# Performance work log

Hardware: AMD Instinct MI355X
Metric: run time of the kernel (lower is better)

## Reference

```python
import jax, jax.numpy as jnp
import numpy as np

N_NODES = 100000
N_EDGES = 2500000


def setup_inputs() -> dict:
    key = jax.random.key(0)
    ks = jax.random.split(key, 13)
    inp = {
        "x": jax.random.normal(ks[0], (N_NODES, 4), dtype=jnp.float32),
        "edge_index": jax.random.randint(ks[1], (2, N_EDGES), 0, N_NODES, dtype=jnp.int64),
        "W_fc1": jax.random.normal(ks[2], (4, 32), dtype=jnp.float32) * 0.5,
        "b_fc1": jax.random.normal(ks[3], (32,), dtype=jnp.float32) * 0.1,
        "W_c1": jax.random.normal(ks[4], (32, 32), dtype=jnp.float32) * (1.0 / np.sqrt(32)),
        "b_c1": jax.random.normal(ks[5], (32,), dtype=jnp.float32) * 0.1,
        "W_c2": jax.random.normal(ks[6], (32, 32), dtype=jnp.float32) * (1.0 / np.sqrt(32)),
        "b_c2": jax.random.normal(ks[7], (32,), dtype=jnp.float32) * 0.1,
        "W_c3": jax.random.normal(ks[8], (32, 32), dtype=jnp.float32) * (1.0 / np.sqrt(32)),
        "b_c3": jax.random.normal(ks[9], (32,), dtype=jnp.float32) * 0.1,
        "W_fc2": jax.random.normal(ks[10], (32, 3), dtype=jnp.float32) * (1.0 / np.sqrt(32)),
        "b_fc2": jax.random.normal(ks[11], (3,), dtype=jnp.float32) * 0.1,
    }
    return inp


def _gcn_norm(edge_index, n_nodes):
    # PyG GCNConv default: add self-loops, symmetric normalization deg^-1/2 A_hat deg^-1/2
    src = jnp.concatenate([edge_index[0], jnp.arange(n_nodes, dtype=edge_index.dtype)])
    dst = jnp.concatenate([edge_index[1], jnp.arange(n_nodes, dtype=edge_index.dtype)])
    deg = jax.ops.segment_sum(jnp.ones_like(dst, dtype=jnp.float32), dst, num_segments=n_nodes)
    dinv = jnp.where(deg > 0, jax.lax.rsqrt(deg), 0.0)
    norm = dinv[src] * dinv[dst]  # [E + N]
    return src, dst, norm


def _gcn_conv(x, src, dst, norm, W, b, n_nodes):
    h = x @ W                                  # [N, 32] small GEMM
    msg = h[src] * norm[:, None]               # gather + scale  [E+N, 32]
    out = jax.ops.segment_sum(msg, dst, num_segments=n_nodes)  # scatter-add
    return out + b


def reference(x, edge_index, W_fc1, b_fc1, W_c1, b_c1, W_c2, b_c2, W_c3, b_c3, W_fc2, b_fc2):
    n_nodes = x.shape[0]
    src, dst, norm = _gcn_norm(edge_index, n_nodes)
    h = jax.nn.relu(x @ W_fc1 + b_fc1)
    h = jax.nn.relu(_gcn_conv(h, src, dst, norm, W_c1, b_c1, n_nodes))
    h = jax.nn.relu(_gcn_conv(h, src, dst, norm, W_c2, b_c2, n_nodes))
    h = jax.nn.relu(_gcn_conv(h, src, dst, norm, W_c3, b_c3, n_nodes))
    return h @ W_fc2 + b_fc2
```

## Files before the change

kernel.cpp:

```cpp
#include <hip/hip_runtime.h>
#include <hip/hip_fp16.h>


constexpr int N_NODES = 100000;
constexpr int N_EDGES = 2500000;
constexpr int QDIV    = 25000;
constexpr int BUCKET  = 256;
constexpr int NBUCK   = (N_NODES + BUCKET - 1) / BUCKET;
constexpr int NBLK    = 512;
constexpr int CHUNK   = (N_EDGES + NBLK - 1) / NBLK;
constexpr int SCAP    = 8192;
constexpr int PERLANE = NBLK / 64;

__global__ __launch_bounds__(256) void k_binfill(const int* __restrict__ ei,
                                                 int* __restrict__ binned,
                                                 int* __restrict__ blkbin,
                                                 int* __restrict__ locoff) {
    __shared__ int cnt[NBUCK];
    __shared__ int cur[NBUCK];
    __shared__ int wsum[4];
    __shared__ int stage[CHUNK];
    __shared__ int payload[CHUNK];
    __shared__ unsigned short binv[CHUNK];
    int tid = threadIdx.x;
    int blk = blockIdx.x;
    int beg = blk * CHUNK;
    int end = min(beg + CHUNK, N_EDGES);
    int m = end - beg;

    for (int i = tid; i < NBUCK; i += 256) cnt[i] = 0;
    __syncthreads();
    for (int e = beg + tid; e < end; e += 256) {
        int sv = ei[e];
        int d  = ei[N_EDGES + e];
        int bin = d >> 8;
        atomicAdd(&cnt[bin], 1);
        int i = e - beg;
        payload[i] = (sv << 8) | (d & 255);
        binv[i] = (unsigned short)bin;
    }
    __syncthreads();

    int c0 = (2 * tid     < NBUCK) ? cnt[2 * tid]     : 0;
    int c1 = (2 * tid + 1 < NBUCK) ? cnt[2 * tid + 1] : 0;
    int s  = c0 + c1;
    int incl = s;
#pragma unroll
    for (int o = 1; o < 64; o <<= 1) {
        int tm = __shfl_up(incl, o);
        if ((tid & 63) >= o) incl += tm;
    }
    if ((tid & 63) == 63) wsum[tid >> 6] = incl;
    __syncthreads();
    int wexcl = 0;
#pragma unroll
    for (int wi = 0; wi < 4; ++wi) wexcl += (wi < (tid >> 6)) ? wsum[wi] : 0;
    int texcl = wexcl + incl - s;
    {
        int i = 2 * tid;
        if (i < NBUCK) {
            cur[i] = texcl;
            blkbin[i * NBLK + blk] = c0;
            locoff[blk * NBUCK + i] = beg + texcl;
        }
        i = 2 * tid + 1;
        if (i < NBUCK) {
            int e1 = texcl + c0;
            cur[i] = e1;
            blkbin[i * NBLK + blk] = c1;
            locoff[blk * NBUCK + i] = beg + e1;
        }
    }
    __syncthreads();

    for (int i = tid; i < m; i += 256) {
        int pos = atomicAdd(&cur[binv[i]], 1);
        stage[pos] = payload[i];
    }
    __syncthreads();
    for (int i = tid; i < m; i += 256) binned[beg + i] = stage[i];
}

__global__ __launch_bounds__(256) void k_binwave(const int* __restrict__ blkbin,
                                                 int* __restrict__ bintot,
                                                 int* __restrict__ blkpos) {
    int w = threadIdx.x >> 6, lane = threadIdx.x & 63;
    int bin = blockIdx.x * 4 + w;
    if (bin >= NBUCK) return;
    int v[PERLANE];
#pragma unroll
    for (int i = 0; i < PERLANE; ++i) v[i] = blkbin[bin * NBLK + lane * PERLANE + i];
    int mysum = 0;
#pragma unroll
    for (int i = 0; i < PERLANE; ++i) mysum += v[i];
    int pre = mysum;
#pragma unroll
    for (int o = 1; o < 64; o <<= 1) {
        int t = __shfl_up(pre, o);
        if (lane >= o) pre += t;
    }
    int excl = pre - mysum;
    int run = excl;
#pragma unroll
    for (int i = 0; i < PERLANE; ++i) {
        blkpos[bin * NBLK + lane * PERLANE + i] = run;
        run += v[i];
    }
    if (lane == 63) bintot[bin] = pre;
}

__global__ __launch_bounds__(512) void k_sortdeg(const int* __restrict__ binned,
                                                 const int* __restrict__ blkbin,
                                                 const int* __restrict__ blkpos,
                                                 const int* __restrict__ locoff,
                                                 const int* __restrict__ bintot,
                                                 unsigned short* __restrict__ csr16,
                                                 int* __restrict__ rowseg,
                                                 float* __restrict__ dinv) {
    __shared__ int stage[SCAP];
    __shared__ unsigned short outs[SCAP];
    __shared__ int runlen[NBLK];
    __shared__ int runpos[NBLK];
    __shared__ int cnt[1024];
    __shared__ int sc[1024];
    __shared__ int cur[1024];
    __shared__ int wred[8];
    __shared__ int wtot[8];
    int t = threadIdx.x;
    int b = blockIdx.x;

    int part = 0;
    for (int i = t; i < b; i += 512) part += bintot[i];
#pragma unroll
    for (int o = 32; o > 0; o >>= 1) part += __shfl_xor(part, o);
    if ((t & 63) == 0) wred[t >> 6] = part;

    if (t < NBLK) {
        runlen[t] = blkbin[b * NBLK + t];
        runpos[t] = blkpos[b * NBLK + t];
    }
    cnt[t] = 0; cnt[t + 512] = 0;
    __syncthreads();

    int beg = 0;
#pragma unroll
    for (int wi = 0; wi < 8; ++wi) beg += wred[wi];
    int end = beg + bintot[b];
    int total = end - beg;
    bool fits = (total <= SCAP);

    if (fits) {
        for (int blk = t; blk < NBLK; blk += 512) {
            int len = runlen[blk];
            int srcp = locoff[blk * NBUCK + b];
            int dstp = runpos[blk];
            int i = 0;
            while (i < len && ((srcp + i) & 3)) { stage[dstp + i] = binned[srcp + i]; ++i; }
            for (; i + 3 < len; i += 4) {
                int4 v = *(const int4*)(binned + srcp + i);
                stage[dstp + i]     = v.x;
                stage[dstp + i + 1] = v.y;
                stage[dstp + i + 2] = v.z;
                stage[dstp + i + 3] = v.w;
            }
            for (; i < len; ++i) stage[dstp + i] = binned[srcp + i];
        }
        __syncthreads();
        for (int k = t; k < total; k += 512) {
            int p = stage[k];
            int key = ((p & 255) << 2) | ((p >> 8) / QDIV);
            atomicAdd(&cnt[key], 1);
        }
    } else {
        for (int blk = t; blk < NBLK; blk += 512) {
            int len = runlen[blk];
            int srcp = locoff[blk * NBUCK + b];
            for (int i = 0; i < len; ++i) {
                int p = binned[srcp + i];
                int key = ((p & 255) << 2) | ((p >> 8) / QDIV);
                atomicAdd(&cnt[key], 1);
            }
        }
    }
    __syncthreads();

    int c0 = cnt[2 * t], c1 = cnt[2 * t + 1];
    int s = c0 + c1;
    int incl = s;
#pragma unroll
    for (int o = 1; o < 64; o <<= 1) {
        int tm = __shfl_up(incl, o);
        if ((t & 63) >= o) incl += tm;
    }
    if ((t & 63) == 63) wtot[t >> 6] = incl;
    __syncthreads();
    int wexcl = 0;
#pragma unroll
    for (int wi = 0; wi < 8; ++wi) wexcl += (wi < (t >> 6)) ? wtot[wi] : 0;
    int texcl = wexcl + incl - s;
    sc[2 * t]     = texcl + c0;
    sc[2 * t + 1] = texcl + s;
    __syncthreads();

#pragma unroll
    for (int slot = 0; slot < 2; ++slot) {
        int k = 2 * t + slot;
        int excl = (slot == 0) ? texcl : (texcl + c0);
        cur[k] = excl;
        int dl = k >> 2, q = k & 3;
        int n = b * BUCKET + dl;
        if (n < N_NODES) {
            rowseg[n * 4 + q] = beg + excl;
            if (q == 0) {
                int deg = sc[k + 3] - excl;
                dinv[n] = rsqrtf((float)(deg + 1));
            }
        }
    }
    if (b == NBUCK - 1 && t == 0) rowseg[(size_t)N_NODES * 4] = end;
    __syncthreads();

    if (fits) {
        for (int k = t; k < total; k += 512) {
            int p = stage[k];
            int src = p >> 8;
            int q = src / QDIV;
            int key = ((p & 255) << 2) | q;
            int pos = atomicAdd(&cur[key], 1);
            outs[pos] = (unsigned short)(src - q * QDIV);
        }
        __syncthreads();
        for (int k = t; k < total; k += 512)
            csr16[beg + k] = outs[k];
    } else {
        for (int blk = t; blk < NBLK; blk += 512) {
            int len = runlen[blk];
            int srcp = locoff[blk * NBUCK + b];
            for (int i = 0; i < len; ++i) {
                int p = binned[srcp + i];
                int src = p >> 8;
                int q = src / QDIV;
                int key = ((p & 255) << 2) | q;
                int pos = atomicAdd(&cur[key], 1);
                csr16[beg + pos] = (unsigned short)(src - q * QDIV);
            }
        }
    }
}

__device__ inline void store_half8(__half* p, const float* v) {
    __half2 h[4];
#pragma unroll
    for (int i = 0; i < 4; ++i)
        h[i] = __floats2half2_rn(v[2 * i], v[2 * i + 1]);
    *(float4*)p = *(float4*)h;
}

__device__ inline void acc_half8(float* acc, float4 raw) {
    __half2* hp = (__half2*)&raw;
#pragma unroll
    for (int i = 0; i < 4; ++i) {
        float2 f = __half22float2(hp[i]);
        acc[2 * i]     += f.x;
        acc[2 * i + 1] += f.y;
    }
}

__global__ __launch_bounds__(256) void k_fc1_conv1(
        const float* __restrict__ x,
        const float* __restrict__ Wfc1, const float* __restrict__ bfc1,
        const float* __restrict__ Wc1, const float* __restrict__ dinv,
        __half* __restrict__ g) {
    __shared__ float  sWf[128];
    __shared__ float  sbf[32];
    __shared__ float4 sW[256];
    if (threadIdx.x < 128) sWf[threadIdx.x] = Wfc1[threadIdx.x];
    if (threadIdx.x < 32)  sbf[threadIdx.x] = bfc1[threadIdx.x];
    sW[threadIdx.x] = ((const float4*)Wc1)[threadIdx.x];
    __syncthreads();

    int n = blockIdx.x * 256 + threadIdx.x;
    if (n >= N_NODES) return;

    float4 xin = *(const float4*)(x + (size_t)n * 4);
    float t[32];
#pragma unroll
    for (int j = 0; j < 32; ++j) {
        float a = fmaf(xin.x, sWf[j], sbf[j]);
        a = fmaf(xin.y, sWf[32 + j], a);
        a = fmaf(xin.z, sWf[64 + j], a);
        a = fmaf(xin.w, sWf[96 + j], a);
        t[j] = fmaxf(a, 0.0f);
    }
    float o[32];
#pragma unroll
    for (int j = 0; j < 32; ++j) o[j] = 0.f;
#pragma unroll
    for (int k = 0; k < 32; ++k) {
        float a = t[k];
#pragma unroll
        for (int q = 0; q < 8; ++q) {
            float4 w = sW[k * 8 + q];
            o[q * 4 + 0] = fmaf(a, w.x, o[q * 4 + 0]);
            o[q * 4 + 1] = fmaf(a, w.y, o[q * 4 + 1]);
            o[q * 4 + 2] = fmaf(a, w.z, o[q * 4 + 2]);
            o[q * 4 + 3] = fmaf(a, w.w, o[q * 4 + 3]);
        }
    }
    float dv = dinv[n];
#pragma unroll
    for (int j = 0; j < 32; ++j) o[j] *= dv;
    __half* gp = g + (size_t)n * 32;
    store_half8(gp,      o);
    store_half8(gp + 8,  o + 8);
    store_half8(gp + 16, o + 16);
    store_half8(gp + 24, o + 24);
}

__device__ inline void gather_seg(int beg, int end, int base,
                                  const unsigned short* __restrict__ csr16,
                                  const __half* __restrict__ gin, int sub, float* acc) {
    int k = beg;
    int stop = beg + ((end - beg) & ~3);
    if (k < stop) {
        int s0 = base + csr16[k],     s1 = base + csr16[k + 1];
        int s2 = base + csr16[k + 2], s3 = base + csr16[k + 3];
        k += 4;
        while (k < stop) {
            float4 r0 = *(const float4*)(gin + (size_t)s0 * 32 + sub * 8);
            float4 r1 = *(const float4*)(gin + (size_t)s1 * 32 + sub * 8);
            float4 r2 = *(const float4*)(gin + (size_t)s2 * 32 + sub * 8);
            float4 r3 = *(const float4*)(gin + (size_t)s3 * 32 + sub * 8);
            s0 = base + csr16[k];     s1 = base + csr16[k + 1];
            s2 = base + csr16[k + 2]; s3 = base + csr16[k + 3];
            acc_half8(acc, r0); acc_half8(acc, r1);
            acc_half8(acc, r2); acc_half8(acc, r3);
            k += 4;
        }
        float4 r0 = *(const float4*)(gin + (size_t)s0 * 32 + sub * 8);
        float4 r1 = *(const float4*)(gin + (size_t)s1 * 32 + sub * 8);
        float4 r2 = *(const float4*)(gin + (size_t)s2 * 32 + sub * 8);
        float4 r3 = *(const float4*)(gin + (size_t)s3 * 32 + sub * 8);
        acc_half8(acc, r0); acc_half8(acc, r1);
        acc_half8(acc, r2); acc_half8(acc, r3);
    }
    for (; k < end; ++k) {
        int s = base + csr16[k];
        float4 r = *(const float4*)(gin + (size_t)s * 32 + sub * 8);
        acc_half8(acc, r);
    }
}

__global__ __launch_bounds__(256) void k_gather_mid(
        const int* __restrict__ rowseg,
        const unsigned short* __restrict__ csr16, const __half* __restrict__ gin,
        const float* __restrict__ dinv,
        const float* __restrict__ b, const float* __restrict__ W,
        __half* __restrict__ gout) {
    __shared__ float sS[64 * 33];
    __shared__ float sW[1024];
    __shared__ float sb[32];
    for (int i = threadIdx.x; i < 1024; i += 256) sW[i] = W[i];
    if (threadIdx.x < 32) sb[threadIdx.x] = b[threadIdx.x];

    int nl = threadIdx.x >> 2;
    int sub = threadIdx.x & 3;
    int n = blockIdx.x * 64 + nl;
    float acc[8];
    if (n < N_NODES) {
        float4 self = *(const float4*)(gin + (size_t)n * 32 + sub * 8);
        {
            __half2* hp = (__half2*)&self;
#pragma unroll
            for (int i = 0; i < 4; ++i) {
                float2 f = __half22float2(hp[i]);
                acc[2 * i] = f.x;
                acc[2 * i + 1] = f.y;
            }
        }
        int4 seg = *(const int4*)(rowseg + (size_t)n * 4);
        int segend = rowseg[(size_t)n * 4 + 4];
        gather_seg(seg.x, seg.y, 0,         csr16, gin, sub, acc);
        gather_seg(seg.y, seg.z, QDIV,      csr16, gin, sub, acc);
        gather_seg(seg.z, seg.w, 2 * QDIV,  csr16, gin, sub, acc);
        gather_seg(seg.w, segend, 3 * QDIV, csr16, gin, sub, acc);
#pragma unroll
        for (int i = 0; i < 8; ++i) sS[nl * 33 + sub * 8 + i] = acc[i];
    }
    __syncthreads();

    if (n >= N_NODES) return;
    float dv = dinv[n];
    float t[32];
#pragma unroll
    for (int kk = 0; kk < 32; ++kk)
        t[kk] = fmaxf(fmaf(dv, sS[nl * 33 + kk], sb[kk]), 0.0f);
    float o[8];
#pragma unroll
    for (int j = 0; j < 8; ++j) o[j] = 0.f;
#pragma unroll
    for (int kk = 0; kk < 32; ++kk) {
        float a = t[kk];
#pragma unroll
        for (int j = 0; j < 8; ++j)
            o[j] = fmaf(a, sW[kk * 32 + sub * 8 + j], o[j]);
    }
#pragma unroll
    for (int j = 0; j < 8; ++j) o[j] *= dv;
    store_half8(gout + (size_t)n * 32 + sub * 8, o);
}

__global__ __launch_bounds__(256) void k_gather_out(
        const int* __restrict__ rowseg,
        const unsigned short* __restrict__ csr16, const __half* __restrict__ gin,
        const float* __restrict__ dinv,
        const float* __restrict__ bc3, const float* __restrict__ Wfc2,
        const float* __restrict__ bfc2, float* __restrict__ out) {
    __shared__ float sS[64 * 33];
    __shared__ float sW[96];
    __shared__ float sb[32];
    __shared__ float sb2[3];
    if (threadIdx.x < 96) sW[threadIdx.x] = Wfc2[threadIdx.x];
    if (threadIdx.x < 32) sb[threadIdx.x] = bc3[threadIdx.x];
    if (threadIdx.x < 3)  sb2[threadIdx.x] = bfc2[threadIdx.x];

    int nl = threadIdx.x >> 2;
    int sub = threadIdx.x & 3;
    int n = blockIdx.x * 64 + nl;
    float acc[8];
    if (n < N_NODES) {
        float4 self = *(const float4*)(gin + (size_t)n * 32 + sub * 8);
        {
            __half2* hp = (__half2*)&self;
#pragma unroll
            for (int i = 0; i < 4; ++i) {
                float2 f = __half22float2(hp[i]);
                acc[2 * i] = f.x;
                acc[2 * i + 1] = f.y;
            }
        }
        int4 seg = *(const int4*)(rowseg + (size_t)n * 4);
        int segend = rowseg[(size_t)n * 4 + 4];
        gather_seg(seg.x, seg.y, 0,         csr16, gin, sub, acc);
        gather_seg(seg.y, seg.z, QDIV,      csr16, gin, sub, acc);
        gather_seg(seg.z, seg.w, 2 * QDIV,  csr16, gin, sub, acc);
        gather_seg(seg.w, segend, 3 * QDIV, csr16, gin, sub, acc);
#pragma unroll
        for (int i = 0; i < 8; ++i) sS[nl * 33 + sub * 8 + i] = acc[i];
    }
    __syncthreads();

    if (n >= N_NODES || sub != 0) return;
    float dv = dinv[n];
    float t[32];
#pragma unroll
    for (int kk = 0; kk < 32; ++kk)
        t[kk] = fmaxf(fmaf(dv, sS[nl * 33 + kk], sb[kk]), 0.0f);
    float o0 = sb2[0], o1 = sb2[1], o2 = sb2[2];
#pragma unroll
    for (int kk = 0; kk < 32; ++kk) {
        o0 = fmaf(t[kk], sW[kk * 3 + 0], o0);
        o1 = fmaf(t[kk], sW[kk * 3 + 1], o1);
        o2 = fmaf(t[kk], sW[kk * 3 + 2], o2);
    }
    out[(size_t)n * 3 + 0] = o0;
    out[(size_t)n * 3 + 1] = o1;
    out[(size_t)n * 3 + 2] = o2;
}

extern "C" void kernel_launch(void* const* d_in, const int* in_sizes, int n_in,
                              void* d_out, int out_size, void* d_ws, size_t ws_size,
                              hipStream_t stream) {
    const float* x    = (const float*)d_in[0];
    const int*   ei   = (const int*)d_in[1];
    const float* Wfc1 = (const float*)d_in[2];
    const float* bfc1 = (const float*)d_in[3];
    const float* Wc1  = (const float*)d_in[4];
    const float* bc1  = (const float*)d_in[5];
    const float* Wc2  = (const float*)d_in[6];
    const float* bc2  = (const float*)d_in[7];
    const float* Wc3  = (const float*)d_in[8];
    const float* bc3  = (const float*)d_in[9];
    const float* Wfc2 = (const float*)d_in[10];
    const float* bfc2 = (const float*)d_in[11];
    float* out = (float*)d_out;

    char* ws = (char*)d_ws;
    const size_t grow = (size_t)N_NODES * 32 * sizeof(__half);
    size_t off = 0;
    __half* gA     = (__half*)(ws + off); off += grow;
    __half* gB     = (__half*)(ws + off); off += grow;
    int*   binned  = (int*)  (ws + off); off += (size_t)NBLK * CHUNK * sizeof(int);
    unsigned short* csr16 = (unsigned short*)(ws + off);
    off += ((size_t)N_EDGES + 8) * sizeof(unsigned short);
    float* dinv    = (float*)(ws + off); off += (size_t)N_NODES * sizeof(float);
    int*   rowseg  = (int*)  (ws + off); off += ((size_t)N_NODES * 4 + 16) * sizeof(int);
    int*   blkbin  = (int*)  (ws + off); off += (size_t)NBUCK * NBLK * sizeof(int);
    int*   blkpos  = (int*)  (ws + off); off += (size_t)NBUCK * NBLK * sizeof(int);
    int*   locoff  = (int*)  (ws + off); off += (size_t)NBLK * NBUCK * sizeof(int);
    int*   bintot  = (int*)  (ws + off); off += (size_t)NBUCK * sizeof(int);

    const int nb_wave = (NBUCK + 3) / 4;
    const int nb_n = (N_NODES + 255) / 256;
    const int nb_f = (N_NODES * 4 + 255) / 256;

    k_binfill<<<NBLK, 256, 0, stream>>>(ei, binned, blkbin, locoff);
    k_binwave<<<nb_wave, 256, 0, stream>>>(blkbin, bintot, blkpos);
    k_sortdeg<<<NBUCK, 512, 0, stream>>>(binned, blkbin, blkpos, locoff, bintot,
                                         csr16, rowseg, dinv);

    k_fc1_conv1<<<nb_n, 256, 0, stream>>>(x, Wfc1, bfc1, Wc1, dinv, gA);
    k_gather_mid<<<nb_f, 256, 0, stream>>>(rowseg, csr16, gA, dinv, bc1, Wc2, gB);
    k_gather_mid<<<nb_f, 256, 0, stream>>>(rowseg, csr16, gB, dinv, bc2, Wc3, gA);
    k_gather_out<<<nb_f, 256, 0, stream>>>(rowseg, csr16, gA, dinv, bc3, Wfc2, bfc2, out);
}
```

Baseline: 205.2 us.

## Remove bin-scan kernel by computing offsets inside sortdeg; vectorize edge loads

```diff
diff --git a/kernel.cpp b/kernel.cpp
--- a/kernel.cpp
+++ b/kernel.cpp
@@ -10,7 +10,7 @@
 constexpr int NBLK    = 512;
 constexpr int CHUNK   = (N_EDGES + NBLK - 1) / NBLK;
 constexpr int SCAP    = 8192;
-constexpr int PERLANE = NBLK / 64;
+constexpr int SUMOFF  = CHUNK * ((NBLK * (NBLK - 1)) / 2);
 
 __global__ __launch_bounds__(256) void k_binfill(const int* __restrict__ ei,
                                                  int* __restrict__ binned,
@@ -30,14 +30,42 @@
 
     for (int i = tid; i < NBUCK; i += 256) cnt[i] = 0;
     __syncthreads();
-    for (int e = beg + tid; e < end; e += 256) {
-        int sv = ei[e];
-        int d  = ei[N_EDGES + e];
+
+    int a0 = min((beg + 3) & ~3, end);
+    int a1 = (end > a0) ? (a0 + ((end - a0) & ~3)) : a0;
+    if (tid < a0 - beg) {
+        int e = beg + tid;
+        int sv = ei[e], d = ei[N_EDGES + e];
         int bin = d >> 8;
         atomicAdd(&cnt[bin], 1);
+        payload[e - beg] = (sv << 8) | (d & 255);
+        binv[e - beg] = (unsigned short)bin;
+    }
+    for (int e = a0 + tid * 4; e < a1; e += 1024) {
+        int4 s4 = *(const int4*)(ei + e);
+        int4 d4 = *(const int4*)(ei + N_EDGES + e);
         int i = e - beg;
-        payload[i] = (sv << 8) | (d & 255);
-        binv[i] = (unsigned short)bin;
+        int b0 = d4.x >> 8, b1 = d4.y >> 8, b2 = d4.z >> 8, b3 = d4.w >> 8;
+        atomicAdd(&cnt[b0], 1); atomicAdd(&cnt[b1], 1);
+        atomicAdd(&cnt[b2], 1); atomicAdd(&cnt[b3], 1);
+        payload[i]     = (s4.x << 8) | (d4.x & 255);
+        payload[i + 1] = (s4.y << 8) | (d4.y & 255);
+        payload[i + 2] = (s4.z << 8) | (d4.z & 255);
+        payload[i + 3] = (s4.w << 8) | (d4.w & 255);
+        binv[i]     = (unsigned short)b0;
+        binv[i + 1] = (unsigned short)b1;
+        binv[i + 2] = (unsigned short)b2;
+        binv[i + 3] = (unsigned short)b3;
+    }
+    {
+        int e = a1 + tid;
+        if (e < end) {
+            int sv = ei[e], d = ei[N_EDGES + e];
+            int bin = d >> 8;
+            atomicAdd(&cnt[bin], 1);
+            payload[e - beg] = (sv << 8) | (d & 255);
+            binv[e - beg] = (unsigned short)bin;
+        }
     }
     __syncthreads();
 
@@ -81,39 +109,9 @@
     for (int i = tid; i < m; i += 256) binned[beg + i] = stage[i];
 }
 
-__global__ __launch_bounds__(256) void k_binwave(const int* __restrict__ blkbin,
-                                                 int* __restrict__ bintot,
-                                                 int* __restrict__ blkpos) {
-    int w = threadIdx.x >> 6, lane = threadIdx.x & 63;
-    int bin = blockIdx.x * 4 + w;
-    if (bin >= NBUCK) return;
-    int v[PERLANE];
-#pragma unroll
-    for (int i = 0; i < PERLANE; ++i) v[i] = blkbin[bin * NBLK + lane * PERLANE + i];
-    int mysum = 0;
-#pragma unroll
-    for (int i = 0; i < PERLANE; ++i) mysum += v[i];
-    int pre = mysum;
-#pragma unroll
-    for (int o = 1; o < 64; o <<= 1) {
-        int t = __shfl_up(pre, o);
-        if (lane >= o) pre += t;
-    }
-    int excl = pre - mysum;
-    int run = excl;
-#pragma unroll
-    for (int i = 0; i < PERLANE; ++i) {
-        blkpos[bin * NBLK + lane * PERLANE + i] = run;
-        run += v[i];
-    }
-    if (lane == 63) bintot[bin] = pre;
-}
-
 __global__ __launch_bounds__(512) void k_sortdeg(const int* __restrict__ binned,
                                                  const int* __restrict__ blkbin,
-                                                 const int* __restrict__ blkpos,
                                                  const int* __restrict__ locoff,
-                                                 const int* __restrict__ bintot,
                                                  unsigned short* __restrict__ csr16,
                                                  int* __restrict__ rowseg,
                                                  float* __restrict__ dinv) {
@@ -121,38 +119,51 @@
     __shared__ unsigned short outs[SCAP];
     __shared__ int runlen[NBLK];
     __shared__ int runpos[NBLK];
+    __shared__ int loc[NBLK];
     __shared__ int cnt[1024];
     __shared__ int sc[1024];
     __shared__ int cur[1024];
-    __shared__ int wred[8];
     __shared__ int wtot[8];
+    __shared__ int wloc[8];
     int t = threadIdx.x;
     int b = blockIdx.x;
-
-    int part = 0;
-    for (int i = t; i < b; i += 512) part += bintot[i];
-#pragma unroll
-    for (int o = 32; o > 0; o >>= 1) part += __shfl_xor(part, o);
-    if ((t & 63) == 0) wred[t >> 6] = part;
-
-    if (t < NBLK) {
-        runlen[t] = blkbin[b * NBLK + t];
-        runpos[t] = blkpos[b * NBLK + t];
-    }
+    int lane = t & 63, w = t >> 6;
+
+    int rl = blkbin[b * NBLK + t];
+    int lc = locoff[t * NBUCK + b];
+    runlen[t] = rl;
+    loc[t] = lc;
     cnt[t] = 0; cnt[t + 512] = 0;
-    __syncthreads();
-
-    int beg = 0;
-#pragma unroll
-    for (int wi = 0; wi < 8; ++wi) beg += wred[wi];
-    int end = beg + bintot[b];
-    int total = end - beg;
+
+    int incl = rl;
+#pragma unroll
+    for (int o = 1; o < 64; o <<= 1) {
+        int tm = __shfl_up(incl, o);
+        if (lane >= o) incl += tm;
+    }
+    int lsum = lc;
+#pragma unroll
+    for (int o = 32; o > 0; o >>= 1) lsum += __shfl_xor(lsum, o);
+    if (lane == 63) wtot[w] = incl;
+    if (lane == 0)  wloc[w] = lsum;
+    __syncthreads();
+    int wexcl = 0, total = 0, locsum = 0;
+#pragma unroll
+    for (int wi = 0; wi < 8; ++wi) {
+        wexcl  += (wi < w) ? wtot[wi] : 0;
+        total  += wtot[wi];
+        locsum += wloc[wi];
+    }
+    runpos[t] = wexcl + incl - rl;
+    int beg = locsum - SUMOFF;
+    int end = beg + total;
     bool fits = (total <= SCAP);
+    __syncthreads();
 
     if (fits) {
         for (int blk = t; blk < NBLK; blk += 512) {
             int len = runlen[blk];
-            int srcp = locoff[blk * NBUCK + b];
+            int srcp = loc[blk];
             int dstp = runpos[blk];
             int i = 0;
             while (i < len && ((srcp + i) & 3)) { stage[dstp + i] = binned[srcp + i]; ++i; }
@@ -174,7 +185,7 @@
     } else {
         for (int blk = t; blk < NBLK; blk += 512) {
             int len = runlen[blk];
-            int srcp = locoff[blk * NBUCK + b];
+            int srcp = loc[blk];
             for (int i = 0; i < len; ++i) {
                 int p = binned[srcp + i];
                 int key = ((p & 255) << 2) | ((p >> 8) / QDIV);
@@ -186,18 +197,18 @@
 
     int c0 = cnt[2 * t], c1 = cnt[2 * t + 1];
     int s = c0 + c1;
-    int incl = s;
+    int incl2 = s;
 #pragma unroll
     for (int o = 1; o < 64; o <<= 1) {
-        int tm = __shfl_up(incl, o);
-        if ((t & 63) >= o) incl += tm;
-    }
-    if ((t & 63) == 63) wtot[t >> 6] = incl;
-    __syncthreads();
-    int wexcl = 0;
-#pragma unroll
-    for (int wi = 0; wi < 8; ++wi) wexcl += (wi < (t >> 6)) ? wtot[wi] : 0;
-    int texcl = wexcl + incl - s;
+        int tm = __shfl_up(incl2, o);
+        if (lane >= o) incl2 += tm;
+    }
+    if (lane == 63) wtot[w] = incl2;
+    __syncthreads();
+    int wexcl2 = 0;
+#pragma unroll
+    for (int wi = 0; wi < 8; ++wi) wexcl2 += (wi < w) ? wtot[wi] : 0;
+    int texcl = wexcl2 + incl2 - s;
     sc[2 * t]     = texcl + c0;
     sc[2 * t + 1] = texcl + s;
     __syncthreads();
@@ -235,7 +246,7 @@
     } else {
         for (int blk = t; blk < NBLK; blk += 512) {
             int len = runlen[blk];
-            int srcp = locoff[blk * NBUCK + b];
+            int srcp = loc[blk];
             for (int i = 0; i < len; ++i) {
                 int p = binned[srcp + i];
                 int src = p >> 8;
@@ -496,17 +507,13 @@
     float* dinv    = (float*)(ws + off); off += (size_t)N_NODES * sizeof(float);
     int*   rowseg  = (int*)  (ws + off); off += ((size_t)N_NODES * 4 + 16) * sizeof(int);
     int*   blkbin  = (int*)  (ws + off); off += (size_t)NBUCK * NBLK * sizeof(int);
-    int*   blkpos  = (int*)  (ws + off); off += (size_t)NBUCK * NBLK * sizeof(int);
     int*   locoff  = (int*)  (ws + off); off += (size_t)NBLK * NBUCK * sizeof(int);
-    int*   bintot  = (int*)  (ws + off); off += (size_t)NBUCK * sizeof(int);
-
-    const int nb_wave = (NBUCK + 3) / 4;
+
     const int nb_n = (N_NODES + 255) / 256;
     const int nb_f = (N_NODES * 4 + 255) / 256;
 
     k_binfill<<<NBLK, 256, 0, stream>>>(ei, binned, blkbin, locoff);
-    k_binwave<<<nb_wave, 256, 0, stream>>>(blkbin, bintot, blkpos);
-    k_sortdeg<<<NBUCK, 512, 0, stream>>>(binned, blkbin, blkpos, locoff, bintot,
+    k_sortdeg<<<NBUCK, 512, 0, stream>>>(binned, blkbin, locoff,
                                          csr16, rowseg, dinv);
 
     k_fc1_conv1<<<nb_n, 256, 0, stream>>>(x, Wfc1, bfc1, Wc1, dinv, gA);
```

Result: faster. 198.8 us (-3.1%).
